# Kernel optimization log

Hardware: AMD Instinct MI355X
Metric: run time of the kernel (lower is better)

## Reference

```python
import jax, jax.numpy as jnp
from jax import lax
import numpy as np

B, T, F, H = 64, 512, 256, 512


def _gru_scan(data_tbf, Wi, bi, Wh, bhn):
    """Run a flax-style GRUCell over time. data_tbf: (T, B, F) -> (T, B, H)."""
    def step(h, x):
        xg = x @ Wi + bi              # (B, 3H): ir | iz | in
        hg = h @ Wh                   # (B, 3H): hr | hz | hn (hn bias added below)
        xr, xz, xn = jnp.split(xg, 3, axis=-1)
        hr, hz, hn = jnp.split(hg, 3, axis=-1)
        r = jax.nn.sigmoid(xr + hr)
        z = jax.nn.sigmoid(xz + hz)
        n = jnp.tanh(xn + r * (hn + bhn))
        new_h = (1.0 - z) * n + z * h
        return new_h, new_h

    h0 = jnp.zeros((data_tbf.shape[1], Wh.shape[0]), data_tbf.dtype)
    _, ys = lax.scan(step, h0, data_tbf)
    return ys


def setup_inputs() -> dict:
    key = jax.random.key(0)
    ks = jax.random.split(key, 5)
    s_i = 1.0 / np.sqrt(F)
    s_h = 1.0 / np.sqrt(H)
    return {
        "data": jax.random.normal(ks[0], (B, T, F), jnp.float32),
        "Wi_f": jax.random.normal(ks[1], (F, 3 * H), jnp.float32) * s_i,
        "bi_f": jnp.zeros((3 * H,), jnp.float32),
        "Wh_f": jax.random.normal(ks[2], (H, 3 * H), jnp.float32) * s_h,
        "bhn_f": jnp.zeros((H,), jnp.float32),
        "Wi_b": jax.random.normal(ks[3], (F, 3 * H), jnp.float32) * s_i,
        "bi_b": jnp.zeros((3 * H,), jnp.float32),
        "Wh_b": jax.random.normal(ks[4], (H, 3 * H), jnp.float32) * s_h,
        "bhn_b": jnp.zeros((H,), jnp.float32),
    }


def reference(data, Wi_f, bi_f, Wh_f, bhn_f, Wi_b, bi_b, Wh_b, bhn_b):
    # Forward direction: scan over time (axis 1 of data)
    fwd = _gru_scan(jnp.swapaxes(data, 0, 1), Wi_f, bi_f, Wh_f, bhn_f)
    fwd = jnp.swapaxes(fwd, 0, 1)                      # (B, T, H)
    # 'Backward' direction: source flips axis 0 (batch), faithfully reproduced.
    rev = jnp.flip(data, axis=0)
    bwd = _gru_scan(jnp.swapaxes(rev, 0, 1), Wi_b, bi_b, Wh_b, bhn_b)
    bwd = jnp.swapaxes(bwd, 0, 1)                      # (B, T, H)
    bwd = jnp.flip(bwd, axis=0)
    return jnp.concatenate([fwd, bwd], axis=-1)        # (B, T, 2H)
```

## Files before the change

kernel.cpp:

```cpp
#include <hip/hip_runtime.h>
#include <hip/hip_bf16.h>


#define TT 512
#define FF 256
#define HH 512
#define G3 1536
#define NWG 256
#define NTHR 64

typedef __attribute__((ext_vector_type(8))) short short8;
typedef __attribute__((ext_vector_type(4))) float f32x4;
typedef unsigned int u32;
typedef unsigned long long u64;

union U4 { uint4 v; u32 u[4]; u64 q[2]; };

__device__ __forceinline__ unsigned short f2bf(float f) {
  union { float f; unsigned u; } x; x.f = f;
  return (unsigned short)((x.u + 0x7fffu + ((x.u >> 16) & 1u)) >> 16);
}

__device__ __forceinline__ unsigned pk2(float a, float b) {
  union { __hip_bfloat162 h; unsigned u; } x;
  x.h = __float22bfloat162_rn(make_float2(a, b));
  return x.u;
}

__device__ __forceinline__ float sigm(float x) {
  return __builtin_amdgcn_rcpf(1.f + __expf(-x));
}

#define MFMA(a, b, c) __builtin_amdgcn_mfma_f32_16x16x32_bf16((a), (b), (c), 0, 0, 0)

__global__ __launch_bounds__(NTHR, 1) void gru_fused(
    const float* __restrict__ data,
    const float* __restrict__ Wi_f, const float* __restrict__ bi_f,
    const float* __restrict__ Wh_f, const float* __restrict__ bhn_f,
    const float* __restrict__ Wi_b, const float* __restrict__ bi_b,
    const float* __restrict__ Wh_b, const float* __restrict__ bhn_b,
    float* __restrict__ out,
    u32* __restrict__ hbuf)
{
  const int wg   = blockIdx.x;
  const int unit = wg & 7;
  const int s    = wg >> 3;
  const int dir  = unit >> 2;
  const int bg   = unit & 3;
  const int lane = threadIdx.x;
  const int l15  = lane & 15;
  const int lg   = lane >> 4;

  const float* Wi  = dir ? Wi_b  : Wi_f;
  const float* Wh  = dir ? Wh_b  : Wh_f;
  const float* bi  = dir ? bi_b  : bi_f;
  const float* bhn = dir ? bhn_b : bhn_f;

  const int colT = s * 16 + l15;
  const int colBase = s * 16 + lg * 4;

  short8 whf[3][16];
#pragma unroll
  for (int g = 0; g < 3; ++g)
#pragma unroll
    for (int ks = 0; ks < 16; ++ks) {
      short8 v;
#pragma unroll
      for (int j = 0; j < 8; ++j)
        v[j] = (short)f2bf(Wh[(size_t)(ks * 32 + lg * 8 + j) * G3 + g * HH + colT]);
      whf[g][ks] = v;
    }
  short8 wif[3][8];
#pragma unroll
  for (int g = 0; g < 3; ++g)
#pragma unroll
    for (int ks = 0; ks < 8; ++ks) {
      short8 v;
#pragma unroll
      for (int j = 0; j < 8; ++j)
        v[j] = (short)f2bf(Wi[(size_t)(ks * 32 + lg * 8 + j) * G3 + g * HH + colT]);
      wif[g][ks] = v;
    }
  float biR[4], biZ[4], biN[4], bhc[4];
#pragma unroll
  for (int j = 0; j < 4; ++j) {
    biR[j] = bi[colBase + j];
    biZ[j] = bi[HH + colBase + j];
    biN[j] = bi[2 * HH + colBase + j];
    bhc[j] = bhn[colBase + j];
  }

  const float* xbase = data + (size_t)(bg * 16 + l15) * TT * FF;
  float hp[4] = {0.f, 0.f, 0.f, 0.f};

  for (int t = 0; t < TT; ++t) {
    f32x4 accR = {0.f, 0.f, 0.f, 0.f};
    f32x4 accZ = {0.f, 0.f, 0.f, 0.f};
    f32x4 xN   = {0.f, 0.f, 0.f, 0.f};
    {
      const float* xr = xbase + (size_t)t * FF;
#pragma unroll
      for (int ks = 0; ks < 8; ++ks) {
        float4 x0 = *(const float4*)(xr + ks * 32 + lg * 8);
        float4 x1 = *(const float4*)(xr + ks * 32 + lg * 8 + 4);
        union { short8 s; unsigned u[4]; } a;
        a.u[0] = pk2(x0.x, x0.y); a.u[1] = pk2(x0.z, x0.w);
        a.u[2] = pk2(x1.x, x1.y); a.u[3] = pk2(x1.z, x1.w);
        accR = MFMA(wif[0][ks], a.s, accR);
        accZ = MFMA(wif[1][ks], a.s, accZ);
        xN   = MFMA(wif[2][ks], a.s, xN);
      }
    }

    const u32 tag = (u32)t;
    const u32* hb = hbuf + ((size_t)(unit * 2 + (t & 1)) << 13);
    U4 q[32];
    while (true) {
#pragma unroll
      for (int ks = 0; ks < 16; ++ks) {
        const u32* p = hb + l15 * 512 + ks * 32 + lg * 8;
        asm volatile("global_load_dwordx4 %0, %1, off sc0 sc1"
                     : "=v"(q[2 * ks].v) : "v"(p));
        asm volatile("global_load_dwordx4 %0, %1, off sc0 sc1"
                     : "=v"(q[2 * ks + 1].v) : "v"(p + 4));
      }
      asm volatile("s_waitcnt vmcnt(0)" ::: "memory");
      u32 bad = 0;
#pragma unroll
      for (int c = 0; c < 32; ++c) {
        bad |= (q[c].u[0] ^ tag) & 0xffffu;
        bad |= (q[c].u[3] ^ tag) & 0xffffu;
      }
      if (__all(bad == 0)) break;
    }

    f32x4 hN = {0.f, 0.f, 0.f, 0.f};
#pragma unroll
    for (int ks = 0; ks < 16; ++ks) {
      union { short8 s; unsigned u[4]; } a;
#pragma unroll
      for (int i = 0; i < 2; ++i) {
        const U4& c = q[2 * ks + i];
        a.u[2 * i]     = __builtin_amdgcn_perm(c.u[1], c.u[0], 0x07060302u);
        a.u[2 * i + 1] = __builtin_amdgcn_perm(c.u[3], c.u[2], 0x07060302u);
      }
      accR = MFMA(whf[0][ks], a.s, accR);
      accZ = MFMA(whf[1][ks], a.s, accZ);
      hN   = MFMA(whf[2][ks], a.s, hN);
    }

    float hv[4];
#pragma unroll
    for (int j = 0; j < 4; ++j) {
      float r = sigm(accR[j] + biR[j]);
      float z = sigm(accZ[j] + biZ[j]);
      float e = __expf(2.f * (xN[j] + biN[j] + r * (hN[j] + bhc[j])));
      float n = 1.f - 2.f * __builtin_amdgcn_rcpf(e + 1.f);
      hv[j] = (1.f - z) * n + z * hp[j];
      hp[j] = hv[j];
    }

    {
      U4 w;
      const u32 wtag = (u32)(t + 1);
#pragma unroll
      for (int j = 0; j < 4; ++j)
        w.u[j] = ((u32)f2bf(hv[j]) << 16) | wtag;
      u32* ho = hbuf + ((size_t)(unit * 2 + ((t + 1) & 1)) << 13);
      u64* pdst = (u64*)(ho + l15 * 512 + s * 16 + lg * 4);
      __hip_atomic_store(&pdst[0], w.q[0], __ATOMIC_RELAXED, __HIP_MEMORY_SCOPE_AGENT);
      __hip_atomic_store(&pdst[1], w.q[1], __ATOMIC_RELAXED, __HIP_MEMORY_SCOPE_AGENT);
    }

    *(float4*)(out + ((size_t)(bg * 16 + l15) * TT + t) * 1024 + (size_t)dir * HH + colBase)
        = make_float4(hv[0], hv[1], hv[2], hv[3]);
  }
}

extern "C" void kernel_launch(void* const* d_in, const int* in_sizes, int n_in,
                              void* d_out, int out_size, void* d_ws, size_t ws_size,
                              hipStream_t stream) {
  const float* data  = (const float*)d_in[0];
  const float* Wi_f  = (const float*)d_in[1];
  const float* bi_f  = (const float*)d_in[2];
  const float* Wh_f  = (const float*)d_in[3];
  const float* bhn_f = (const float*)d_in[4];
  const float* Wi_b  = (const float*)d_in[5];
  const float* bi_b  = (const float*)d_in[6];
  const float* Wh_b  = (const float*)d_in[7];
  const float* bhn_b = (const float*)d_in[8];
  float* out = (float*)d_out;

  u32* hbuf = (u32*)d_ws;
  (void)hipMemsetAsync(d_ws, 0, 524288, stream);

  gru_fused<<<NWG, NTHR, 0, stream>>>(data, Wi_f, bi_f, Wh_f, bhn_f,
                                      Wi_b, bi_b, Wh_b, bhn_b, out, hbuf);
}
```

Before: 3.747 ms.

## Poll hidden state through a local-scope buffer with periodic global-coherent fallback

Duplicates the inter-workgroup hidden-state exchange buffer into two copies. One copy is written with workgroup-scope stores and polled with sc0-only loads, which may be served from a nearer cache level. The other copy is written with agent-scope stores and polled with sc0 sc1 loads, used on odd iterations after the fourth failed poll. The aim is to cut polling latency in the per-timestep spin barrier. The cost is doubled store traffic and reliance on cache coherence behavior for the local copy, with the global copy as the correctness fallback.

```diff
diff --git a/kernel.cpp b/kernel.cpp
--- a/kernel.cpp
+++ b/kernel.cpp
@@ -40,7 +40,8 @@
     const float* __restrict__ Wi_b, const float* __restrict__ bi_b,
     const float* __restrict__ Wh_b, const float* __restrict__ bhn_b,
     float* __restrict__ out,
-    u32* __restrict__ hbuf)
+    u32* __restrict__ hbufL,
+    u32* __restrict__ hbufG)
 {
   const int wg   = blockIdx.x;
   const int unit = wg & 7;
@@ -113,16 +114,31 @@
     }
 
     const u32 tag = (u32)t;
-    const u32* hb = hbuf + ((size_t)(unit * 2 + (t & 1)) << 13);
+    const size_t boff = (size_t)(unit * 2 + (t & 1)) << 13;
+    const u32* hbL = hbufL + boff;
+    const u32* hbG = hbufG + boff;
     U4 q[32];
+    int it = 0;
     while (true) {
-#pragma unroll
-      for (int ks = 0; ks < 16; ++ks) {
-        const u32* p = hb + l15 * 512 + ks * 32 + lg * 8;
-        asm volatile("global_load_dwordx4 %0, %1, off sc0 sc1"
-                     : "=v"(q[2 * ks].v) : "v"(p));
-        asm volatile("global_load_dwordx4 %0, %1, off sc0 sc1"
-                     : "=v"(q[2 * ks + 1].v) : "v"(p + 4));
+      const bool llc = (it >= 4) && (it & 1);
+      if (llc) {
+#pragma unroll
+        for (int ks = 0; ks < 16; ++ks) {
+          const u32* p = hbG + l15 * 512 + ks * 32 + lg * 8;
+          asm volatile("global_load_dwordx4 %0, %1, off sc0 sc1"
+                       : "=v"(q[2 * ks].v) : "v"(p));
+          asm volatile("global_load_dwordx4 %0, %1, off sc0 sc1"
+                       : "=v"(q[2 * ks + 1].v) : "v"(p + 4));
+        }
+      } else {
+#pragma unroll
+        for (int ks = 0; ks < 16; ++ks) {
+          const u32* p = hbL + l15 * 512 + ks * 32 + lg * 8;
+          asm volatile("global_load_dwordx4 %0, %1, off sc0"
+                       : "=v"(q[2 * ks].v) : "v"(p));
+          asm volatile("global_load_dwordx4 %0, %1, off sc0"
+                       : "=v"(q[2 * ks + 1].v) : "v"(p + 4));
+        }
       }
       asm volatile("s_waitcnt vmcnt(0)" ::: "memory");
       u32 bad = 0;
@@ -132,6 +148,7 @@
         bad |= (q[c].u[3] ^ tag) & 0xffffu;
       }
       if (__all(bad == 0)) break;
+      ++it;
     }
 
     f32x4 hN = {0.f, 0.f, 0.f, 0.f};
@@ -166,10 +183,14 @@
 #pragma unroll
       for (int j = 0; j < 4; ++j)
         w.u[j] = ((u32)f2bf(hv[j]) << 16) | wtag;
-      u32* ho = hbuf + ((size_t)(unit * 2 + ((t + 1) & 1)) << 13);
-      u64* pdst = (u64*)(ho + l15 * 512 + s * 16 + lg * 4);
-      __hip_atomic_store(&pdst[0], w.q[0], __ATOMIC_RELAXED, __HIP_MEMORY_SCOPE_AGENT);
-      __hip_atomic_store(&pdst[1], w.q[1], __ATOMIC_RELAXED, __HIP_MEMORY_SCOPE_AGENT);
+      const size_t ooff = ((size_t)(unit * 2 + ((t + 1) & 1)) << 13)
+                        + l15 * 512 + s * 16 + lg * 4;
+      u64* pL = (u64*)(hbufL + ooff);
+      u64* pG = (u64*)(hbufG + ooff);
+      __hip_atomic_store(&pL[0], w.q[0], __ATOMIC_RELAXED, __HIP_MEMORY_SCOPE_WORKGROUP);
+      __hip_atomic_store(&pL[1], w.q[1], __ATOMIC_RELAXED, __HIP_MEMORY_SCOPE_WORKGROUP);
+      __hip_atomic_store(&pG[0], w.q[0], __ATOMIC_RELAXED, __HIP_MEMORY_SCOPE_AGENT);
+      __hip_atomic_store(&pG[1], w.q[1], __ATOMIC_RELAXED, __HIP_MEMORY_SCOPE_AGENT);
     }
 
     *(float4*)(out + ((size_t)(bg * 16 + l15) * TT + t) * 1024 + (size_t)dir * HH + colBase)
@@ -191,9 +212,10 @@
   const float* bhn_b = (const float*)d_in[8];
   float* out = (float*)d_out;
 
-  u32* hbuf = (u32*)d_ws;
-  (void)hipMemsetAsync(d_ws, 0, 524288, stream);
+  u32* hbufL = (u32*)d_ws;
+  u32* hbufG = (u32*)((char*)d_ws + 524288);
+  (void)hipMemsetAsync(d_ws, 0, 1048576, stream);
 
   gru_fused<<<NWG, NTHR, 0, stream>>>(data, Wi_f, bi_f, Wh_f, bhn_f,
-                                      Wi_b, bi_b, Wh_b, bhn_b, out, hbuf);
-}
+                                      Wi_b, bi_b, Wh_b, bhn_b, out, hbufL, hbufG);
+}
```

Measured after the change: 5.030 ms. +34.2%, slower.
